# Optimization experiments

Measured on AMD Instinct MI355X. Metric: run time of the kernel, lower is better.

## Reference

```python
import jax, jax.numpy as jnp
import numpy as np

B, T, D, MP = 32, 256, 512, 20


def setup_inputs() -> dict:
    key = jax.random.key(0)
    k1, k2, k3 = jax.random.split(key, 3)
    reps_lt = jax.random.normal(k1, (B, T, D), dtype=jnp.float32)
    reps_rt = jax.random.normal(k2, (B, T, D), dtype=jnp.float32)
    kernel = jax.random.normal(k3, (1, 1, 1, MP, D), dtype=jnp.float32)
    return {"reps_lt": reps_lt, "reps_rt": reps_rt, "kernel": kernel}


def reference(reps_lt, reps_rt, kernel):
    # kernel: (1,1,1,m,d) -> (m,d)
    km = kernel.reshape(kernel.shape[-2], kernel.shape[-1])
    # scores[b,t,s,m] = sum_d lt[b,t,d] * km[m,d] * rt[b,s,d]
    # matches original broadcast-multiply + sum over d (cosine_norm=False path)
    scores = jnp.einsum('btd,md,bsd->btsm', reps_lt, km, reps_rt)
    match = jnp.tanh(scores)               # [b, t1, t2, m]
    return jnp.max(match, axis=2)          # max-pool over t2 -> [b, t1, m]
```

## Files before the change

### kernel.cpp

```cpp
#include <hip/hip_runtime.h>


constexpr int TT = 256;
constexpr int DD = 512;
constexpr int NM = 20;
constexpr int NB = 32;
constexpr int BM = 64;

typedef float f32x4 __attribute__((ext_vector_type(4)));
typedef int   i32x8 __attribute__((ext_vector_type(8)));

__device__ __forceinline__ unsigned pack_bf16(float lo, float hi) {
    unsigned ulo = __builtin_bit_cast(unsigned, lo);
    unsigned uhi = __builtin_bit_cast(unsigned, hi);
    return (ulo >> 16) | (uhi & 0xFFFF0000u);
}

__device__ __forceinline__ unsigned pk4_fp8(float a, float b, float c, float d) {
    unsigned r = __builtin_amdgcn_cvt_pk_fp8_f32(a, b, 0, false);
    return __builtin_amdgcn_cvt_pk_fp8_f32(c, d, r, true);
}

__global__ __launch_bounds__(256)
void cast_rt(const float* __restrict__ rt, unsigned char* __restrict__ rtf)
{
    const int bid = (int)blockIdx.x;
    const int c8  = bid & 7;
    const int i   = bid >> 3;
    const int b   = c8 + 8 * (i & 3);
    const int sub = i >> 2;
    const int tid = threadIdx.x;
    const int lane = tid & 63;
    const int u6  = sub * 4 + (tid >> 6);
    const int s   = (u6 & 15) * 16 + (lane & 15);
    const int d0  = (u6 >> 4) * 128 + (lane >> 4) * 32;

    const float* p = rt + ((size_t)b * TT + s) * DD + d0;
    float4 x0 = *(const float4*)p;
    float4 x1 = *(const float4*)(p + 4);
    float4 x2 = *(const float4*)(p + 8);
    float4 x3 = *(const float4*)(p + 12);
    float4 x4 = *(const float4*)(p + 16);
    float4 x5 = *(const float4*)(p + 20);
    float4 x6 = *(const float4*)(p + 24);
    float4 x7 = *(const float4*)(p + 28);
    uint4 w0, w1;
    w0.x = pk4_fp8(x0.x, x0.y, x0.z, x0.w);
    w0.y = pk4_fp8(x1.x, x1.y, x1.z, x1.w);
    w0.z = pk4_fp8(x2.x, x2.y, x2.z, x2.w);
    w0.w = pk4_fp8(x3.x, x3.y, x3.z, x3.w);
    w1.x = pk4_fp8(x4.x, x4.y, x4.z, x4.w);
    w1.y = pk4_fp8(x5.x, x5.y, x5.z, x5.w);
    w1.z = pk4_fp8(x6.x, x6.y, x6.z, x6.w);
    w1.w = pk4_fp8(x7.x, x7.y, x7.z, x7.w);
    unsigned char* dst = rtf + ((size_t)b * 4096 + (size_t)u6 * 64 + lane) * 32;
    *(uint4*)dst        = w0;
    *(uint4*)(dst + 16) = w1;
}

__global__ __launch_bounds__(512, 4)
void mp_match_mx(const float* __restrict__ lt, const unsigned char* __restrict__ rtf,
                 const float* __restrict__ km, float* __restrict__ out)
{
    __shared__ __attribute__((aligned(32))) uint4 Ash[BM * 34];
    __shared__ __attribute__((aligned(16))) float maxbuf[8][BM];

    const int f  = blockIdx.x;
    const int c8 = f & 7;
    const int i  = f >> 3;
    const int b  = c8 + 8 * (i / 80);
    const int j  = i % 80;
    const int m  = j >> 2;
    const int t0 = (j & 3) * BM;

    const int tid  = threadIdx.x;
    const int w    = tid >> 6;
    const int lane = tid & 63;
    const int l15  = lane & 15;
    const int l4   = lane >> 4;

    const float* ltB = lt + ((size_t)b * TT + t0) * DD;
    const float* kmp = km + (size_t)m * DD;
    const unsigned char* rtB0 = rtf + (size_t)b * 131072 + (size_t)(w * 128 + lane) * 32;

    i32x8 ring[2];
    auto loadB = [&](int u) {
        ring[u & 1] = *(const i32x8*)(rtB0 + (u >> 1) * 32768 + (u & 1) * 2048);
    };

    loadB(0);

    {
        const int cc8 = tid & 63;
        const int r0  = (tid >> 6) * 8;
        const float* kp = kmp + cc8 * 8;
        const float4 k0 = *(const float4*)(kp);
        const float4 k1 = *(const float4*)(kp + 4);
#pragma unroll
        for (int r = 0; r < 8; ++r) {
            const float* src = ltB + (size_t)(r0 + r) * DD + cc8 * 8;
            float4 x0 = *(const float4*)src;
            float4 x1 = *(const float4*)(src + 4);
            uint2 o;
            o.x = pk4_fp8(x0.x * k0.x, x0.y * k0.y, x0.z * k0.z, x0.w * k0.w);
            o.y = pk4_fp8(x1.x * k1.x, x1.y * k1.y, x1.z * k1.z, x1.w * k1.w);
            unsigned* cell = (unsigned*)&Ash[(r0 + r) * 34 + (cc8 >> 1)];
            *(uint2*)(cell + (cc8 & 1) * 2) = o;
        }
    }
    __syncthreads();

    f32x4 acc[4][2] = {};
    i32x8 av[4];

#pragma unroll
    for (int u = 0; u < 8; ++u) {
        const int kk = u >> 1, jj = u & 1;
        if (u + 1 < 8) loadB(u + 1);
        if (jj == 0) {
#pragma unroll
            for (int ii = 0; ii < 4; ++ii)
                av[ii] = *(const i32x8*)&Ash[(ii * 16 + l15) * 34 + kk * 8 + l4 * 2];
        }
        const i32x8 bv = ring[u & 1];
#pragma unroll
        for (int ii = 0; ii < 4; ++ii)
            acc[ii][jj] = __builtin_amdgcn_mfma_scale_f32_16x16x128_f8f6f4(
                av[ii], bv, acc[ii][jj], 0, 0, 0, 127, 0, 127);
    }

#pragma unroll
    for (int ii = 0; ii < 4; ++ii) {
        f32x4 v = acc[ii][0];
        v.x = fmaxf(v.x, acc[ii][1].x);
        v.y = fmaxf(v.y, acc[ii][1].y);
        v.z = fmaxf(v.z, acc[ii][1].z);
        v.w = fmaxf(v.w, acc[ii][1].w);
#pragma unroll
        for (int off = 1; off < 16; off <<= 1) {
            v.x = fmaxf(v.x, __shfl_xor(v.x, off, 64));
            v.y = fmaxf(v.y, __shfl_xor(v.y, off, 64));
            v.z = fmaxf(v.z, __shfl_xor(v.z, off, 64));
            v.w = fmaxf(v.w, __shfl_xor(v.w, off, 64));
        }
        if (l15 == 0)
            *(f32x4*)&maxbuf[w][ii * 16 + l4 * 4] = v;
    }
    __syncthreads();
    if (tid < BM) {
        float v0 = fmaxf(fmaxf(maxbuf[0][tid], maxbuf[1][tid]),
                         fmaxf(maxbuf[2][tid], maxbuf[3][tid]));
        float v1 = fmaxf(fmaxf(maxbuf[4][tid], maxbuf[5][tid]),
                         fmaxf(maxbuf[6][tid], maxbuf[7][tid]));
        out[((size_t)b * TT + t0 + tid) * NM + m] = tanhf(fmaxf(v0, v1));
    }
}

typedef short bf16x8 __attribute__((ext_vector_type(8)));

__global__ __launch_bounds__(256, 2)
void mp_match_kernel(const float* __restrict__ lt, const float* __restrict__ rt,
                     const float* __restrict__ km, float* __restrict__ out)
{
    __shared__ __attribute__((aligned(16))) unsigned short Ash[2][4][128][8];
    __shared__ __attribute__((aligned(16))) unsigned short Bsh2[2][4][256][8];
    __shared__ __attribute__((aligned(16))) float maxbuf[2][128];

    const int ttile = blockIdx.x, m = blockIdx.y, b = blockIdx.z;
    const int t0 = ttile * 128;
    const int tid = threadIdx.x, wave = tid >> 6, lane = tid & 63;
    const int l15 = lane & 15, l4 = lane >> 4;
    const int wt = (wave & 1) * 64, wsi = wave >> 1;

    const float* ltp = lt + ((size_t)b * TT + t0) * DD;
    const float* rtp = rt + (size_t)b * TT * DD;
    const float* kmp = km + (size_t)m * DD;
    const int a_t = tid >> 1, a_h = tid & 1;

    f32x4 acc[4][8] = {};

    auto stage = [&](int kk, int buf) {
        const int d0 = kk * 32;
        const float* ap = ltp + (size_t)a_t * DD + d0 + a_h * 16;
        const float* kp = kmp + d0 + a_h * 16;
#pragma unroll
        for (int q = 0; q < 2; ++q) {
            float4 x0 = *(const float4*)(ap + q * 8);
            float4 x1 = *(const float4*)(ap + q * 8 + 4);
            float4 k0 = *(const float4*)(kp + q * 8);
            float4 k1 = *(const float4*)(kp + q * 8 + 4);
            uint4 wv;
            wv.x = pack_bf16(x0.x * k0.x, x0.y * k0.y);
            wv.y = pack_bf16(x0.z * k0.z, x0.w * k0.w);
            wv.z = pack_bf16(x1.x * k1.x, x1.y * k1.y);
            wv.w = pack_bf16(x1.z * k1.z, x1.w * k1.w);
            *(uint4*)&Ash[buf][a_h * 2 + q][a_t][0] = wv;
        }
        const float* bp = rtp + (size_t)tid * DD + d0;
#pragma unroll
        for (int p = 0; p < 4; ++p) {
            float4 y0 = *(const float4*)(bp + p * 8);
            float4 y1 = *(const float4*)(bp + p * 8 + 4);
            uint4 wv;
            wv.x = pack_bf16(y0.x, y0.y);
            wv.y = pack_bf16(y0.z, y0.w);
            wv.z = pack_bf16(y1.x, y1.y);
            wv.w = pack_bf16(y1.z, y1.w);
            *(uint4*)&Bsh2[buf][p][tid][0] = wv;
        }
    };

    stage(0, 0);
    for (int kk = 0; kk < 16; ++kk) {
        const int buf = kk & 1;
        __syncthreads();
        bf16x8 af[4], bfv[8];
#pragma unroll
        for (int i2 = 0; i2 < 4; ++i2)
            af[i2] = *(const bf16x8*)&Ash[buf][l4][wt + i2 * 16 + l15][0];
#pragma unroll
        for (int j2 = 0; j2 < 8; ++j2)
            bfv[j2] = *(const bf16x8*)&Bsh2[buf][l4][wsi * 128 + j2 * 16 + l15][0];
        if (kk + 1 < 16) stage(kk + 1, buf ^ 1);
#pragma unroll
        for (int i2 = 0; i2 < 4; ++i2)
#pragma unroll
            for (int j2 = 0; j2 < 8; ++j2)
                acc[i2][j2] = __builtin_amdgcn_mfma_f32_16x16x32_bf16(af[i2], bfv[j2], acc[i2][j2], 0, 0, 0);
    }
#pragma unroll
    for (int i2 = 0; i2 < 4; ++i2) {
        f32x4 v = acc[i2][0];
#pragma unroll
        for (int j2 = 1; j2 < 8; ++j2) {
            v.x = fmaxf(v.x, acc[i2][j2].x); v.y = fmaxf(v.y, acc[i2][j2].y);
            v.z = fmaxf(v.z, acc[i2][j2].z); v.w = fmaxf(v.w, acc[i2][j2].w);
        }
#pragma unroll
        for (int off = 1; off < 16; off <<= 1) {
            v.x = fmaxf(v.x, __shfl_xor(v.x, off, 64));
            v.y = fmaxf(v.y, __shfl_xor(v.y, off, 64));
            v.z = fmaxf(v.z, __shfl_xor(v.z, off, 64));
            v.w = fmaxf(v.w, __shfl_xor(v.w, off, 64));
        }
        if (l15 == 0) *(f32x4*)&maxbuf[wsi][wt + i2 * 16 + l4 * 4] = v;
    }
    __syncthreads();
    if (tid < 128) {
        float v = fmaxf(maxbuf[0][tid], maxbuf[1][tid]);
        out[((size_t)b * TT + t0 + tid) * NM + m] = tanhf(v);
    }
}

extern "C" void kernel_launch(void* const* d_in, const int* in_sizes, int n_in,
                              void* d_out, int out_size, void* d_ws, size_t ws_size,
                              hipStream_t stream) {
    const float* lt  = (const float*)d_in[0];
    const float* rt  = (const float*)d_in[1];
    const float* km  = (const float*)d_in[2];
    float*       out = (float*)d_out;

    const size_t elems = (size_t)NB * TT * DD;
    const size_t rtfB  = elems;

    if (ws_size >= rtfB) {
        unsigned char* rtf = (unsigned char*)d_ws;
        cast_rt<<<512, 256, 0, stream>>>(rt, rtf);
        mp_match_mx<<<2560, 512, 0, stream>>>(lt, rtf, km, out);
    } else {
        mp_match_kernel<<<dim3(2, NM, NB), 256, 0, stream>>>(lt, rt, km, out);
    }
}
```

Baseline: 113.0 us.

## Precompute scaled fp8 lt tiles in pre-pass and load via direct global-to-LDS

Moves the lt*km scaling and fp8 conversion into a combined cast kernel that writes a per-(batch, perspective, tile) swizzled fp8 buffer. The matching kernel then fills shared memory with async global-to-LDS loads instead of converting fp32 in-kernel. It also deepens the B register ring to three stages. This removes conversion ALU work and LDS write latency from the MFMA kernel, but materialises a large 20x-expanded workspace that must be written and reread, and it requires a much bigger workspace.

```diff
diff --git a/kernel.cpp b/kernel.cpp
--- a/kernel.cpp
+++ b/kernel.cpp
@@ -21,48 +21,99 @@
     return __builtin_amdgcn_cvt_pk_fp8_f32(c, d, r, true);
 }
 
+__device__ __forceinline__ void gld_lds16(const void* g, void* l) {
+    __builtin_amdgcn_global_load_lds(
+        (const __attribute__((address_space(1))) void*)g,
+        (__attribute__((address_space(3))) void*)l, 16, 0, 0);
+}
+
 __global__ __launch_bounds__(256)
-void cast_rt(const float* __restrict__ rt, unsigned char* __restrict__ rtf)
+void cast_ops(const float* __restrict__ lt, const float* __restrict__ rt,
+              const float* __restrict__ km,
+              unsigned char* __restrict__ ltf, unsigned char* __restrict__ rtf)
 {
     const int bid = (int)blockIdx.x;
-    const int c8  = bid & 7;
-    const int i   = bid >> 3;
-    const int b   = c8 + 8 * (i & 3);
-    const int sub = i >> 2;
     const int tid = threadIdx.x;
-    const int lane = tid & 63;
-    const int u6  = sub * 4 + (tid >> 6);
-    const int s   = (u6 & 15) * 16 + (lane & 15);
-    const int d0  = (u6 >> 4) * 128 + (lane >> 4) * 32;
-
-    const float* p = rt + ((size_t)b * TT + s) * DD + d0;
-    float4 x0 = *(const float4*)p;
-    float4 x1 = *(const float4*)(p + 4);
-    float4 x2 = *(const float4*)(p + 8);
-    float4 x3 = *(const float4*)(p + 12);
-    float4 x4 = *(const float4*)(p + 16);
-    float4 x5 = *(const float4*)(p + 20);
-    float4 x6 = *(const float4*)(p + 24);
-    float4 x7 = *(const float4*)(p + 28);
-    uint4 w0, w1;
-    w0.x = pk4_fp8(x0.x, x0.y, x0.z, x0.w);
-    w0.y = pk4_fp8(x1.x, x1.y, x1.z, x1.w);
-    w0.z = pk4_fp8(x2.x, x2.y, x2.z, x2.w);
-    w0.w = pk4_fp8(x3.x, x3.y, x3.z, x3.w);
-    w1.x = pk4_fp8(x4.x, x4.y, x4.z, x4.w);
-    w1.y = pk4_fp8(x5.x, x5.y, x5.z, x5.w);
-    w1.z = pk4_fp8(x6.x, x6.y, x6.z, x6.w);
-    w1.w = pk4_fp8(x7.x, x7.y, x7.z, x7.w);
-    unsigned char* dst = rtf + ((size_t)b * 4096 + (size_t)u6 * 64 + lane) * 32;
-    *(uint4*)dst        = w0;
-    *(uint4*)(dst + 16) = w1;
+    if (bid < 10240) {
+        const int c8  = bid & 7;
+        const int g   = bid >> 3;
+        const int b   = c8 + 8 * (g & 3);
+        const int sub = g >> 2;
+        const int m   = sub >> 4;
+        const int q   = sub & 15;
+        const int ti  = q >> 2;
+        const int row = (q & 3) * 16 + (tid >> 4);
+        const int c   = tid & 15;
+        const int d0  = c * 32;
+
+        const float* lp = lt + (((size_t)b * TT + ti * BM + row) * DD + d0);
+        const float* kp = km + (size_t)m * DD + d0;
+        uint4 w0, w1;
+        {
+            float4 x0 = *(const float4*)(lp);      float4 k0 = *(const float4*)(kp);
+            float4 x1 = *(const float4*)(lp + 4);  float4 k1 = *(const float4*)(kp + 4);
+            float4 x2 = *(const float4*)(lp + 8);  float4 k2 = *(const float4*)(kp + 8);
+            float4 x3 = *(const float4*)(lp + 12); float4 k3 = *(const float4*)(kp + 12);
+            w0.x = pk4_fp8(x0.x * k0.x, x0.y * k0.y, x0.z * k0.z, x0.w * k0.w);
+            w0.y = pk4_fp8(x1.x * k1.x, x1.y * k1.y, x1.z * k1.z, x1.w * k1.w);
+            w0.z = pk4_fp8(x2.x * k2.x, x2.y * k2.y, x2.z * k2.z, x2.w * k2.w);
+            w0.w = pk4_fp8(x3.x * k3.x, x3.y * k3.y, x3.z * k3.z, x3.w * k3.w);
+        }
+        {
+            float4 x0 = *(const float4*)(lp + 16); float4 k0 = *(const float4*)(kp + 16);
+            float4 x1 = *(const float4*)(lp + 20); float4 k1 = *(const float4*)(kp + 20);
+            float4 x2 = *(const float4*)(lp + 24); float4 k2 = *(const float4*)(kp + 24);
+            float4 x3 = *(const float4*)(lp + 28); float4 k3 = *(const float4*)(kp + 28);
+            w1.x = pk4_fp8(x0.x * k0.x, x0.y * k0.y, x0.z * k0.z, x0.w * k0.w);
+            w1.y = pk4_fp8(x1.x * k1.x, x1.y * k1.y, x1.z * k1.z, x1.w * k1.w);
+            w1.z = pk4_fp8(x2.x * k2.x, x2.y * k2.y, x2.z * k2.z, x2.w * k2.w);
+            w1.w = pk4_fp8(x3.x * k3.x, x3.y * k3.y, x3.z * k3.z, x3.w * k3.w);
+        }
+        const size_t tbase = (((size_t)b * NM + m) * 4 + ti) * 32768;
+        const int    lbyte = (row * 512 + c * 32) ^ ((row & 3) << 5);
+        unsigned char* dst = ltf + tbase + lbyte;
+        *(uint4*)dst        = w0;
+        *(uint4*)(dst + 16) = w1;
+    } else {
+        const int bid2 = bid - 10240;
+        const int c8   = bid2 & 7;
+        const int i    = bid2 >> 3;
+        const int b    = c8 + 8 * (i & 3);
+        const int sub  = i >> 2;
+        const int lane = tid & 63;
+        const int u6   = sub * 4 + (tid >> 6);
+        const int s    = (u6 & 15) * 16 + (lane & 15);
+        const int d0   = (u6 >> 4) * 128 + (lane >> 4) * 32;
+
+        const float* p = rt + ((size_t)b * TT + s) * DD + d0;
+        float4 x0 = *(const float4*)p;
+        float4 x1 = *(const float4*)(p + 4);
+        float4 x2 = *(const float4*)(p + 8);
+        float4 x3 = *(const float4*)(p + 12);
+        float4 x4 = *(const float4*)(p + 16);
+        float4 x5 = *(const float4*)(p + 20);
+        float4 x6 = *(const float4*)(p + 24);
+        float4 x7 = *(const float4*)(p + 28);
+        uint4 w0, w1;
+        w0.x = pk4_fp8(x0.x, x0.y, x0.z, x0.w);
+        w0.y = pk4_fp8(x1.x, x1.y, x1.z, x1.w);
+        w0.z = pk4_fp8(x2.x, x2.y, x2.z, x2.w);
+        w0.w = pk4_fp8(x3.x, x3.y, x3.z, x3.w);
+        w1.x = pk4_fp8(x4.x, x4.y, x4.z, x4.w);
+        w1.y = pk4_fp8(x5.x, x5.y, x5.z, x5.w);
+        w1.z = pk4_fp8(x6.x, x6.y, x6.z, x6.w);
+        w1.w = pk4_fp8(x7.x, x7.y, x7.z, x7.w);
+        unsigned char* dst = rtf + ((size_t)b * 4096 + (size_t)u6 * 64 + lane) * 32;
+        *(uint4*)dst        = w0;
+        *(uint4*)(dst + 16) = w1;
+    }
 }
 
 __global__ __launch_bounds__(512, 4)
-void mp_match_mx(const float* __restrict__ lt, const unsigned char* __restrict__ rtf,
-                 const float* __restrict__ km, float* __restrict__ out)
+void mp_match_mx(const unsigned char* __restrict__ ltf, const unsigned char* __restrict__ rtf,
+                 float* __restrict__ out)
 {
-    __shared__ __attribute__((aligned(32))) uint4 Ash[BM * 34];
+    __shared__ __attribute__((aligned(16))) uint4 Ash[2048];
     __shared__ __attribute__((aligned(16))) float maxbuf[8][BM];
 
     const int f  = blockIdx.x;
@@ -71,7 +122,7 @@
     const int b  = c8 + 8 * (i / 80);
     const int j  = i % 80;
     const int m  = j >> 2;
-    const int t0 = (j & 3) * BM;
+    const int ti = j & 3;
 
     const int tid  = threadIdx.x;
     const int w    = tid >> 6;
@@ -79,35 +130,21 @@
     const int l15  = lane & 15;
     const int l4   = lane >> 4;
 
-    const float* ltB = lt + ((size_t)b * TT + t0) * DD;
-    const float* kmp = km + (size_t)m * DD;
+    const unsigned char* aG   = ltf + (((size_t)b * NM + m) * 4 + ti) * 32768;
     const unsigned char* rtB0 = rtf + (size_t)b * 131072 + (size_t)(w * 128 + lane) * 32;
 
-    i32x8 ring[2];
+#pragma unroll
+    for (int r = 0; r < 4; ++r) {
+        const int off = w * 4096 + r * 1024 + lane * 16;
+        gld_lds16(aG + off, (char*)Ash + off);
+    }
+
+    i32x8 ring[3];
     auto loadB = [&](int u) {
-        ring[u & 1] = *(const i32x8*)(rtB0 + (u >> 1) * 32768 + (u & 1) * 2048);
+        ring[u % 3] = *(const i32x8*)(rtB0 + (u >> 1) * 32768 + (u & 1) * 2048);
     };
-
-    loadB(0);
-
-    {
-        const int cc8 = tid & 63;
-        const int r0  = (tid >> 6) * 8;
-        const float* kp = kmp + cc8 * 8;
-        const float4 k0 = *(const float4*)(kp);
-        const float4 k1 = *(const float4*)(kp + 4);
-#pragma unroll
-        for (int r = 0; r < 8; ++r) {
-            const float* src = ltB + (size_t)(r0 + r) * DD + cc8 * 8;
-            float4 x0 = *(const float4*)src;
-            float4 x1 = *(const float4*)(src + 4);
-            uint2 o;
-            o.x = pk4_fp8(x0.x * k0.x, x0.y * k0.y, x0.z * k0.z, x0.w * k0.w);
-            o.y = pk4_fp8(x1.x * k1.x, x1.y * k1.y, x1.z * k1.z, x1.w * k1.w);
-            unsigned* cell = (unsigned*)&Ash[(r0 + r) * 34 + (cc8 >> 1)];
-            *(uint2*)(cell + (cc8 & 1) * 2) = o;
-        }
-    }
+    loadB(0); loadB(1);
+
     __syncthreads();
 
     f32x4 acc[4][2] = {};
@@ -116,13 +153,15 @@
 #pragma unroll
     for (int u = 0; u < 8; ++u) {
         const int kk = u >> 1, jj = u & 1;
-        if (u + 1 < 8) loadB(u + 1);
+        if (u + 2 < 8) loadB(u + 2);
         if (jj == 0) {
 #pragma unroll
-            for (int ii = 0; ii < 4; ++ii)
-                av[ii] = *(const i32x8*)&Ash[(ii * 16 + l15) * 34 + kk * 8 + l4 * 2];
-        }
-        const i32x8 bv = ring[u & 1];
+            for (int ii = 0; ii < 4; ++ii) {
+                const int lbyte = (((ii * 16 + l15) * 512) + (kk * 4 + l4) * 32) ^ ((l15 & 3) << 5);
+                av[ii] = *(const i32x8*)((const char*)Ash + lbyte);
+            }
+        }
+        const i32x8 bv = ring[u % 3];
 #pragma unroll
         for (int ii = 0; ii < 4; ++ii)
             acc[ii][jj] = __builtin_amdgcn_mfma_scale_f32_16x16x128_f8f6f4(
@@ -152,7 +191,7 @@
                          fmaxf(maxbuf[2][tid], maxbuf[3][tid]));
         float v1 = fmaxf(fmaxf(maxbuf[4][tid], maxbuf[5][tid]),
                          fmaxf(maxbuf[6][tid], maxbuf[7][tid]));
-        out[((size_t)b * TT + t0 + tid) * NM + m] = tanhf(fmaxf(v0, v1));
+        out[((size_t)b * TT + ti * BM + tid) * NM + m] = tanhf(fmaxf(v0, v1));
     }
 }
 
@@ -260,13 +299,13 @@
     const float* km  = (const float*)d_in[2];
     float*       out = (float*)d_out;
 
-    const size_t elems = (size_t)NB * TT * DD;
-    const size_t rtfB  = elems;
-
-    if (ws_size >= rtfB) {
-        unsigned char* rtf = (unsigned char*)d_ws;
-        cast_rt<<<512, 256, 0, stream>>>(rt, rtf);
-        mp_match_mx<<<2560, 512, 0, stream>>>(lt, rtf, km, out);
+    const size_t ltfB = (size_t)NB * NM * TT * DD;
+    const size_t rtfB = (size_t)NB * TT * DD;
+    if (ws_size >= ltfB + rtfB) {
+        unsigned char* ltf = (unsigned char*)d_ws;
+        unsigned char* rtf = (unsigned char*)d_ws + ltfB;
+        cast_ops<<<10752, 256, 0, stream>>>(lt, rt, km, ltf, rtf);
+        mp_match_mx<<<2560, 512, 0, stream>>>(ltf, rtf, out);
     } else {
         mp_match_kernel<<<dim3(2, NM, NB), 256, 0, stream>>>(lt, rt, km, out);
     }
```

After: 189.8 us. 68.0% more time.

## Loop over all perspectives per block, keeping rt fragments and lt rows in registers

Applied to the files above, without the earlier changes.

Each block now handles one batch and a 32-row t tile and loops over all 20 perspectives internally. The rt fp8 fragments are loaded once into registers, and the lt rows are held as packed bf16 in registers; each perspective only rescales those rows by the kernel vector into swizzled LDS. The goal is to cut the repeated global and L2 reads of rt and lt that came from 2560 independent blocks. The cost is a grid of only 256 blocks with serial per-m phases, two barriers per iteration, lower occupancy, and an extra bf16 rounding of lt before the fp8 quantisation.

```diff
diff --git a/kernel.cpp b/kernel.cpp
--- a/kernel.cpp
+++ b/kernel.cpp
@@ -5,7 +5,6 @@
 constexpr int DD = 512;
 constexpr int NM = 20;
 constexpr int NB = 32;
-constexpr int BM = 64;
 
 typedef float f32x4 __attribute__((ext_vector_type(4)));
 typedef int   i32x8 __attribute__((ext_vector_type(8)));
@@ -15,6 +14,8 @@
     unsigned uhi = __builtin_bit_cast(unsigned, hi);
     return (ulo >> 16) | (uhi & 0xFFFF0000u);
 }
+__device__ __forceinline__ float blo(unsigned u) { return __builtin_bit_cast(float, u << 16); }
+__device__ __forceinline__ float bhi(unsigned u) { return __builtin_bit_cast(float, u); }
 
 __device__ __forceinline__ unsigned pk4_fp8(float a, float b, float c, float d) {
     unsigned r = __builtin_amdgcn_cvt_pk_fp8_f32(a, b, 0, false);
@@ -58,20 +59,17 @@
     *(uint4*)(dst + 16) = w1;
 }
 
-__global__ __launch_bounds__(512, 4)
+__global__ __launch_bounds__(512, 2)
 void mp_match_mx(const float* __restrict__ lt, const unsigned char* __restrict__ rtf,
                  const float* __restrict__ km, float* __restrict__ out)
 {
-    __shared__ __attribute__((aligned(32))) uint4 Ash[BM * 34];
-    __shared__ __attribute__((aligned(16))) float maxbuf[8][BM];
+    __shared__ __attribute__((aligned(16))) unsigned char Ash[32 * 512];
+    __shared__ __attribute__((aligned(16))) float maxbuf[8][32];
 
     const int f  = blockIdx.x;
     const int c8 = f & 7;
-    const int i  = f >> 3;
-    const int b  = c8 + 8 * (i / 80);
-    const int j  = i % 80;
-    const int m  = j >> 2;
-    const int t0 = (j & 3) * BM;
+    const int b  = c8 + 8 * ((f >> 3) & 3);
+    const int ti = f >> 5;
 
     const int tid  = threadIdx.x;
     const int w    = tid >> 6;
@@ -79,80 +77,95 @@
     const int l15  = lane & 15;
     const int l4   = lane >> 4;
 
-    const float* ltB = lt + ((size_t)b * TT + t0) * DD;
-    const float* kmp = km + (size_t)m * DD;
     const unsigned char* rtB0 = rtf + (size_t)b * 131072 + (size_t)(w * 128 + lane) * 32;
-
-    i32x8 ring[2];
-    auto loadB = [&](int u) {
-        ring[u & 1] = *(const i32x8*)(rtB0 + (u >> 1) * 32768 + (u & 1) * 2048);
-    };
-
-    loadB(0);
-
+    i32x8 Breg[8];
+#pragma unroll
+    for (int kk = 0; kk < 4; ++kk)
+#pragma unroll
+        for (int jj = 0; jj < 2; ++jj)
+            Breg[kk * 2 + jj] = *(const i32x8*)(rtB0 + kk * 32768 + jj * 2048);
+
+    const int row = tid >> 4, c = tid & 15;
+    unsigned ltp[16];
     {
-        const int cc8 = tid & 63;
-        const int r0  = (tid >> 6) * 8;
-        const float* kp = kmp + cc8 * 8;
-        const float4 k0 = *(const float4*)(kp);
-        const float4 k1 = *(const float4*)(kp + 4);
-#pragma unroll
-        for (int r = 0; r < 8; ++r) {
-            const float* src = ltB + (size_t)(r0 + r) * DD + cc8 * 8;
-            float4 x0 = *(const float4*)src;
-            float4 x1 = *(const float4*)(src + 4);
-            uint2 o;
-            o.x = pk4_fp8(x0.x * k0.x, x0.y * k0.y, x0.z * k0.z, x0.w * k0.w);
-            o.y = pk4_fp8(x1.x * k1.x, x1.y * k1.y, x1.z * k1.z, x1.w * k1.w);
-            unsigned* cell = (unsigned*)&Ash[(r0 + r) * 34 + (cc8 >> 1)];
-            *(uint2*)(cell + (cc8 & 1) * 2) = o;
-        }
-    }
-    __syncthreads();
-
-    f32x4 acc[4][2] = {};
-    i32x8 av[4];
-
-#pragma unroll
-    for (int u = 0; u < 8; ++u) {
-        const int kk = u >> 1, jj = u & 1;
-        if (u + 1 < 8) loadB(u + 1);
-        if (jj == 0) {
-#pragma unroll
-            for (int ii = 0; ii < 4; ++ii)
-                av[ii] = *(const i32x8*)&Ash[(ii * 16 + l15) * 34 + kk * 8 + l4 * 2];
-        }
-        const i32x8 bv = ring[u & 1];
-#pragma unroll
-        for (int ii = 0; ii < 4; ++ii)
-            acc[ii][jj] = __builtin_amdgcn_mfma_scale_f32_16x16x128_f8f6f4(
-                av[ii], bv, acc[ii][jj], 0, 0, 0, 127, 0, 127);
-    }
-
-#pragma unroll
-    for (int ii = 0; ii < 4; ++ii) {
-        f32x4 v = acc[ii][0];
-        v.x = fmaxf(v.x, acc[ii][1].x);
-        v.y = fmaxf(v.y, acc[ii][1].y);
-        v.z = fmaxf(v.z, acc[ii][1].z);
-        v.w = fmaxf(v.w, acc[ii][1].w);
-#pragma unroll
-        for (int off = 1; off < 16; off <<= 1) {
-            v.x = fmaxf(v.x, __shfl_xor(v.x, off, 64));
-            v.y = fmaxf(v.y, __shfl_xor(v.y, off, 64));
-            v.z = fmaxf(v.z, __shfl_xor(v.z, off, 64));
-            v.w = fmaxf(v.w, __shfl_xor(v.w, off, 64));
-        }
-        if (l15 == 0)
-            *(f32x4*)&maxbuf[w][ii * 16 + l4 * 4] = v;
-    }
-    __syncthreads();
-    if (tid < BM) {
-        float v0 = fmaxf(fmaxf(maxbuf[0][tid], maxbuf[1][tid]),
-                         fmaxf(maxbuf[2][tid], maxbuf[3][tid]));
-        float v1 = fmaxf(fmaxf(maxbuf[4][tid], maxbuf[5][tid]),
-                         fmaxf(maxbuf[6][tid], maxbuf[7][tid]));
-        out[((size_t)b * TT + t0 + tid) * NM + m] = tanhf(fmaxf(v0, v1));
+        const float* lp = lt + ((size_t)b * TT + ti * 32 + row) * DD + c * 32;
+#pragma unroll
+        for (int q = 0; q < 8; ++q) {
+            float4 x = *(const float4*)(lp + q * 4);
+            ltp[q * 2]     = pack_bf16(x.x, x.y);
+            ltp[q * 2 + 1] = pack_bf16(x.z, x.w);
+        }
+    }
+    unsigned char* dstA = Ash + row * 512 + (c ^ (row & 15)) * 32;
+
+#pragma unroll 1
+    for (int m = 0; m < NM; ++m) {
+        {
+            const float* kp = km + (size_t)m * DD + c * 32;
+            const float4 kA = *(const float4*)(kp);
+            const float4 kB = *(const float4*)(kp + 4);
+            const float4 kC = *(const float4*)(kp + 8);
+            const float4 kD = *(const float4*)(kp + 12);
+            uint4 o;
+            o.x = pk4_fp8(blo(ltp[0]) * kA.x, bhi(ltp[0]) * kA.y, blo(ltp[1]) * kA.z, bhi(ltp[1]) * kA.w);
+            o.y = pk4_fp8(blo(ltp[2]) * kB.x, bhi(ltp[2]) * kB.y, blo(ltp[3]) * kB.z, bhi(ltp[3]) * kB.w);
+            o.z = pk4_fp8(blo(ltp[4]) * kC.x, bhi(ltp[4]) * kC.y, blo(ltp[5]) * kC.z, bhi(ltp[5]) * kC.w);
+            o.w = pk4_fp8(blo(ltp[6]) * kD.x, bhi(ltp[6]) * kD.y, blo(ltp[7]) * kD.z, bhi(ltp[7]) * kD.w);
+            *(uint4*)dstA = o;
+            const float4 kE = *(const float4*)(kp + 16);
+            const float4 kF = *(const float4*)(kp + 20);
+            const float4 kG = *(const float4*)(kp + 24);
+            const float4 kH = *(const float4*)(kp + 28);
+            o.x = pk4_fp8(blo(ltp[8])  * kE.x, bhi(ltp[8])  * kE.y, blo(ltp[9])  * kE.z, bhi(ltp[9])  * kE.w);
+            o.y = pk4_fp8(blo(ltp[10]) * kF.x, bhi(ltp[10]) * kF.y, blo(ltp[11]) * kF.z, bhi(ltp[11]) * kF.w);
+            o.z = pk4_fp8(blo(ltp[12]) * kG.x, bhi(ltp[12]) * kG.y, blo(ltp[13]) * kG.z, bhi(ltp[13]) * kG.w);
+            o.w = pk4_fp8(blo(ltp[14]) * kH.x, bhi(ltp[14]) * kH.y, blo(ltp[15]) * kH.z, bhi(ltp[15]) * kH.w);
+            *(uint4*)(dstA + 16) = o;
+        }
+        __syncthreads();
+
+        f32x4 acc[2][2] = {};
+#pragma unroll
+        for (int kk = 0; kk < 4; ++kk) {
+            i32x8 av[2];
+#pragma unroll
+            for (int ii = 0; ii < 2; ++ii) {
+                const int r2 = ii * 16 + l15;
+                av[ii] = *(const i32x8*)(Ash + r2 * 512 + (((kk * 4 + l4) ^ l15) * 32));
+            }
+#pragma unroll
+            for (int ii = 0; ii < 2; ++ii)
+#pragma unroll
+                for (int jj = 0; jj < 2; ++jj)
+                    acc[ii][jj] = __builtin_amdgcn_mfma_scale_f32_16x16x128_f8f6f4(
+                        av[ii], Breg[kk * 2 + jj], acc[ii][jj], 0, 0, 0, 127, 0, 127);
+        }
+
+#pragma unroll
+        for (int ii = 0; ii < 2; ++ii) {
+            f32x4 v = acc[ii][0];
+            v.x = fmaxf(v.x, acc[ii][1].x);
+            v.y = fmaxf(v.y, acc[ii][1].y);
+            v.z = fmaxf(v.z, acc[ii][1].z);
+            v.w = fmaxf(v.w, acc[ii][1].w);
+#pragma unroll
+            for (int off = 1; off < 16; off <<= 1) {
+                v.x = fmaxf(v.x, __shfl_xor(v.x, off, 64));
+                v.y = fmaxf(v.y, __shfl_xor(v.y, off, 64));
+                v.z = fmaxf(v.z, __shfl_xor(v.z, off, 64));
+                v.w = fmaxf(v.w, __shfl_xor(v.w, off, 64));
+            }
+            if (l15 == 0)
+                *(f32x4*)&maxbuf[w][ii * 16 + l4 * 4] = v;
+        }
+        __syncthreads();
+        if (tid < 32) {
+            float v0 = fmaxf(fmaxf(maxbuf[0][tid], maxbuf[1][tid]),
+                             fmaxf(maxbuf[2][tid], maxbuf[3][tid]));
+            float v1 = fmaxf(fmaxf(maxbuf[4][tid], maxbuf[5][tid]),
+                             fmaxf(maxbuf[6][tid], maxbuf[7][tid]));
+            out[((size_t)b * TT + ti * 32 + tid) * NM + m] = tanhf(fmaxf(v0, v1));
+        }
     }
 }
 
@@ -260,13 +273,11 @@
     const float* km  = (const float*)d_in[2];
     float*       out = (float*)d_out;
 
-    const size_t elems = (size_t)NB * TT * DD;
-    const size_t rtfB  = elems;
-
+    const size_t rtfB = (size_t)NB * TT * DD;
     if (ws_size >= rtfB) {
         unsigned char* rtf = (unsigned char*)d_ws;
         cast_rt<<<512, 256, 0, stream>>>(rt, rtf);
-        mp_match_mx<<<2560, 512, 0, stream>>>(lt, rtf, km, out);
+        mp_match_mx<<<256, 512, 0, stream>>>(lt, rtf, km, out);
     } else {
         mp_match_kernel<<<dim3(2, NM, NB), 256, 0, stream>>>(lt, rt, km, out);
     }
```

Measured after the change: 149.1 us. +32.0%, slower.
